# Optimization experiments

Hardware: AMD Instinct MI355X
Metric: run time of the kernel (lower is better)

Reference implementation:

```python
import jax, jax.numpy as jnp
import numpy as np

N = 100000   # nodes
E = 800000   # edges (avg degree 8)
IN = 128     # in_dim
H = 128      # hidden_dim
L = 3        # num_layers
EPS = 1e-5   # torch LayerNorm default


def setup_inputs() -> dict:
    key = jax.random.key(0)
    ks = jax.random.split(key, 10)
    s = 0.05
    # DAG edge list: src < dst guarantees acyclicity and node N-1 is a sink.
    rng = np.random.default_rng(0)
    src = rng.integers(0, N - 1, size=E)
    dst = src + 1 + (rng.random(E) * (N - 1 - src)).astype(np.int64)
    return {
        "node_feats": jax.random.normal(ks[0], (N, IN), jnp.float32),
        "src": jnp.asarray(src, jnp.int32),
        "dst": jnp.asarray(dst, jnp.int32),
        "W_in": jax.random.normal(ks[1], (IN, H), jnp.float32) * s,
        "b_in": jnp.zeros((H,), jnp.float32),
        "Ws": jax.random.normal(ks[2], (L, H, H), jnp.float32) * s,
        "bs": jnp.zeros((L, H), jnp.float32),
        "Wn": jax.random.normal(ks[3], (L, H, H), jnp.float32) * s,
        "bn": jnp.zeros((L, H), jnp.float32),
        "Wg": jax.random.normal(ks[4], (L, 2 * H, H), jnp.float32) * s,
        "bg": jnp.zeros((L, H), jnp.float32),
        "gamma": jnp.ones((L, H), jnp.float32),
        "beta": jnp.zeros((L, H), jnp.float32),
        "W_att": jax.random.normal(ks[5], (H, H), jnp.float32) * s,
        "b_att": jnp.zeros((H,), jnp.float32),
        "W_score": jax.random.normal(ks[6], (H, 1), jnp.float32) * s,
        "b_score": jnp.zeros((1,), jnp.float32),
    }


def reference(node_feats, src, dst, W_in, b_in, Ws, bs, Wn, bn, Wg, bg,
              gamma, beta, W_att, b_att, W_score, b_score):
    n = node_feats.shape[0]
    ones_e = jnp.ones(src.shape, node_feats.dtype)
    indeg = jax.ops.segment_sum(ones_e, dst, num_segments=n)          # [N]
    has_pred = (indeg > 0).astype(node_feats.dtype)[:, None]          # [N,1]
    inv_deg = (1.0 / jnp.maximum(indeg, 1.0))[:, None]                # [N,1]
    outdeg = jax.ops.segment_sum(ones_e, src, num_segments=n)
    sink_mask = outdeg == 0                                           # [N]

    h = node_feats @ W_in + b_in                                      # [N,H]
    for i in range(Ws.shape[0]):
        hs = h @ Ws[i] + bs[i]
        # predecessor mean of layer-input h (no within-layer recurrence)
        neigh = jax.ops.segment_sum(h[src], dst, num_segments=n) * inv_deg
        hn = neigh @ Wn[i] + bn[i]
        m = hs + has_pred * hn  # nodes with no preds use m = hs only (bias too)
        gate = jax.nn.sigmoid(jnp.concatenate([h, m], axis=-1) @ Wg[i] + bg[i])
        v = gate * m + (1.0 - gate) * h
        mu = v.mean(-1, keepdims=True)
        var = ((v - mu) ** 2).mean(-1, keepdims=True)
        v = (v - mu) * jax.lax.rsqrt(var + EPS) * gamma[i] + beta[i]
        h = jax.nn.relu(v)

    # attention pooling over sink nodes only
    a = jnp.tanh(h @ W_att + b_att)
    scores = (a @ W_score)[:, 0] + b_score[0]
    scores = jnp.where(sink_mask, scores, -jnp.inf)
    w = jax.nn.softmax(scores, axis=0)  # zero weight on non-sinks
    graph_emb = (w[:, None] * h).sum(0)
    return h, graph_emb
```

## Files before the change

kernel.cpp:

```cpp
#include <hip/hip_runtime.h>
#include <cmath>

typedef unsigned short u16;
typedef unsigned int   u32;
typedef __attribute__((ext_vector_type(8))) short bf16x8;
typedef __attribute__((ext_vector_type(4))) float f32x4;
typedef __attribute__((ext_vector_type(4))) u32   u32x4;

__device__ __forceinline__ float bf2f(u16 u){
    union { u32 i; float f; } x; x.i = ((u32)u) << 16; return x.f;
}
__device__ __forceinline__ u16 f2bf(float f){
    union { float f; u32 i; } x; x.f = f;
    u32 r = x.i + 0x7fffu + ((x.i >> 16) & 1u);
    return (u16)(r >> 16);
}


__global__ void k_count(const int* __restrict__ src, const int* __restrict__ dst,
                        int* cnt, int* notsink, int* pos, int E){
    int e = blockIdx.x*256 + threadIdx.x;
    if (e < E){
        pos[e] = atomicAdd(&cnt[dst[e]], 1);
        notsink[src[e]] = 1;
    }
}

__global__ void k_scan1(const int* __restrict__ in, int* blocksum, int N){
    __shared__ int sh[256];
    int tid = threadIdx.x;
    int base = blockIdx.x*1024 + tid*4;
    int s = 0;
    for (int j=0;j<4;j++){ int i = base+j; s += (i < N) ? in[i] : 0; }
    sh[tid] = s; __syncthreads();
    for (int d=128; d>0; d>>=1){ if (tid < d) sh[tid] += sh[tid+d]; __syncthreads(); }
    if (tid == 0) blocksum[blockIdx.x] = sh[0];
}

__global__ void k_scan2(int* blocksum, int nb){
    if (threadIdx.x == 0){
        int run = 0;
        for (int i=0;i<nb;i++){ int v = blocksum[i]; blocksum[i] = run; run += v; }
    }
}

__global__ void k_scan3(const int* __restrict__ in, const int* __restrict__ blockoff,
                        int* out, float* inv_deg, float* haspred, int N){
    __shared__ int sh[256];
    int tid = threadIdx.x;
    int base = blockIdx.x*1024 + tid*4;
    int e[4]; int s = 0;
    for (int j=0;j<4;j++){ int i = base+j; e[j] = (i < N) ? in[i] : 0; s += e[j]; }
    sh[tid] = s; __syncthreads();
    for (int d=1; d<256; d<<=1){
        int t = (tid >= d) ? sh[tid-d] : 0;
        __syncthreads();
        sh[tid] += t;
        __syncthreads();
    }
    int excl = sh[tid] - s + blockoff[blockIdx.x];
    for (int j=0;j<4;j++){
        int i = base+j;
        if (i < N){
            out[i] = excl; excl += e[j];
            inv_deg[i] = 1.0f / (float)(e[j] > 1 ? e[j] : 1);
            haspred[i] = e[j] > 0 ? 1.0f : 0.0f;
        }
    }
}

__global__ void k_place(const int* __restrict__ src, const int* __restrict__ dst,
                        const int* __restrict__ row_ptr, const int* __restrict__ pos,
                        int* csr_src, int E){
    int e = blockIdx.x*256 + threadIdx.x;
    if (e < E)
        csr_src[row_ptr[dst[e]] + pos[e]] = src[e];
}

__global__ void k_wt(const float* __restrict__ in, u16* __restrict__ out,
                     int shift, int K, int total){
    int i = blockIdx.x*256 + threadIdx.x;
    if (i < total){
        int mat = i >> shift;
        int within = i & ((1 << shift) - 1);
        int k = within >> 7, n = within & 127;
        out[(size_t)mat*(K*128) + n*K + k] = f2bf(in[i]);
    }
}


__global__ void k_neigh(const u16* __restrict__ h, const int* __restrict__ row_ptr,
                        const int* __restrict__ indeg, const float* __restrict__ inv_deg,
                        const int* __restrict__ csr_src, u16* __restrict__ neigh, int N){
    int wid  = (blockIdx.x*256 + threadIdx.x) >> 6;
    int lane = threadIdx.x & 63;
    int sub = lane >> 4, sl = lane & 15;
    int node = wid*4 + sub;
    bool valid = node < N;
    int deg   = valid ? indeg[node]   : 0;
    int start = valid ? row_ptr[node] : 0;
    float acc[8] = {0.f,0.f,0.f,0.f,0.f,0.f,0.f,0.f};
    for (int e0 = 0; __any(e0 < deg); e0 += 16){
        int idx = 0;
        if (e0 + sl < deg) idx = csr_src[start + e0 + sl];
        int cnt = deg - e0;
        #pragma unroll
        for (int j = 0; j < 16; j++){
            int sidx = __shfl(idx, (sub << 4) | j);
            if (j < cnt){
                bf16x8 v = *(const bf16x8*)(h + (size_t)sidx*128 + sl*8);
                #pragma unroll
                for (int t=0;t<8;t++) acc[t] += bf2f((u16)v[t]);
            }
        }
    }
    if (valid){
        float iv = inv_deg[node];
        u16 o[8];
        #pragma unroll
        for (int t=0;t<8;t++) o[t] = f2bf(acc[t]*iv);
        *(u32x4*)(neigh + (size_t)node*128 + sl*8) = *(const u32x4*)o;
    }
}


__device__ __forceinline__ void stage_A_bf16(const u16* __restrict__ A, u16 (*lA)[136],
                                             int row0, int n_rows, int tid){
    #pragma unroll
    for (int i=0;i<4;i++){
        int c = i*256 + tid;
        int r = c >> 4, col8 = (c & 15) * 8;
        u32x4 v = {0,0,0,0};
        if (row0 + r < n_rows)
            v = *(const u32x4*)(A + (size_t)(row0 + r)*128 + col8);
        *(u32x4*)&lA[r][col8] = v;
    }
}

__device__ __forceinline__ void stage_A_f32(const float* __restrict__ A, u16 (*lA)[136],
                                            int row0, int n_rows, int tid){
    #pragma unroll
    for (int i=0;i<4;i++){
        int c = i*256 + tid;
        int r = c >> 4, col8 = (c & 15) * 8;
        u16 o[8] = {0,0,0,0,0,0,0,0};
        if (row0 + r < n_rows){
            float4 v0 = *(const float4*)(A + (size_t)(row0 + r)*128 + col8);
            float4 v1 = *(const float4*)(A + (size_t)(row0 + r)*128 + col8 + 4);
            o[0]=f2bf(v0.x); o[1]=f2bf(v0.y); o[2]=f2bf(v0.z); o[3]=f2bf(v0.w);
            o[4]=f2bf(v1.x); o[5]=f2bf(v1.y); o[6]=f2bf(v1.z); o[7]=f2bf(v1.w);
        }
        *(u32x4*)&lA[r][col8] = *(const u32x4*)o;
    }
}

__device__ __forceinline__ void stage_B(const u16* __restrict__ BT, int Ks, int koff0,
                                        u16 (*lB)[136], int tid){
    #pragma unroll
    for (int i=0;i<8;i++){
        int c = i*256 + tid;
        int n = c >> 4, col8 = (c & 15) * 8;
        u32x4 v = *(const u32x4*)(BT + (size_t)n*Ks + koff0 + col8);
        *(u32x4*)&lB[n][col8] = v;
    }
}

__device__ __forceinline__ void stage_B_half(const u16* __restrict__ BT, int Ks, int koff0,
                                             u16 (*lB)[72], int tid){
    #pragma unroll
    for (int i=0;i<4;i++){
        int c = i*256 + tid;
        int n = c >> 3, col8 = (c & 7) * 8;
        *(u32x4*)&lB[n][col8] = *(const u32x4*)(BT + (size_t)n*Ks + koff0 + col8);
    }
}

__device__ __forceinline__ void mfma_tile(const u16 (*lA)[136], const u16 (*lB)[136],
                                          int wave, int lane, f32x4* acc){
    #pragma unroll
    for (int kk=0;kk<4;kk++){
        int koff = kk*32 + (lane >> 4) * 8;
        bf16x8 a = *(const bf16x8*)&lA[wave*16 + (lane & 15)][koff];
        #pragma unroll
        for (int t=0;t<8;t++){
            bf16x8 b = *(const bf16x8*)&lB[t*16 + (lane & 15)][koff];
            acc[t] = __builtin_amdgcn_mfma_f32_16x16x32_bf16(a, b, acc[t], 0, 0, 0);
        }
    }
}

__device__ __forceinline__ void mfma_half(const u16 (*lA)[136], const u16 (*lB)[72],
                                          int wave, int lane, int kbaseA, f32x4* acc){
    #pragma unroll
    for (int kk=0;kk<2;kk++){
        int kw = kk*32 + (lane >> 4) * 8;
        bf16x8 a = *(const bf16x8*)&lA[wave*16 + (lane & 15)][kbaseA + kw];
        #pragma unroll
        for (int t=0;t<8;t++){
            bf16x8 b = *(const bf16x8*)&lB[t*16 + (lane & 15)][kw];
            acc[t] = __builtin_amdgcn_mfma_f32_16x16x32_bf16(a, b, acc[t], 0, 0, 0);
        }
    }
}


__global__ __launch_bounds__(256) void k_gemm_in(
    const float* __restrict__ A, const u16* __restrict__ BT,
    const float* __restrict__ bias, u16* __restrict__ C, int n_rows)
{
    __shared__ u16 lA[64][136];
    __shared__ u16 lB[128][136];
    int tid = threadIdx.x, wave = tid >> 6, lane = tid & 63;
    int row0 = blockIdx.x * 64;
    f32x4 acc[8];
    #pragma unroll
    for (int t=0;t<8;t++) acc[t] = (f32x4){0.f,0.f,0.f,0.f};
    stage_A_f32(A, lA, row0, n_rows, tid);
    stage_B(BT, 128, 0, lB, tid);
    __syncthreads();
    mfma_tile(lA, lB, wave, lane, acc);

    int sl = lane & 15;
    int rbase = wave*16 + (lane >> 4)*4;
    float bc[8];
    #pragma unroll
    for (int t=0;t<8;t++) bc[t] = bias[t*16 + sl];
    for (int r=0;r<4;r++){
        int row = row0 + rbase + r;
        if (row >= n_rows) continue;
        #pragma unroll
        for (int t=0;t<8;t++)
            C[(size_t)row*128 + t*16 + sl] = f2bf(acc[t][r] + bc[t]);
    }
}


__global__ __launch_bounds__(256) void k_layer(
    const u16* __restrict__ H, const u16* __restrict__ Ng,
    const u16* __restrict__ BsT, const u16* __restrict__ BnT,
    const u16* __restrict__ BgT,
    const float* __restrict__ bs, const float* __restrict__ bn,
    const float* __restrict__ bg,
    const float* __restrict__ gamma, const float* __restrict__ beta,
    const float* __restrict__ haspred,
    u16* __restrict__ Hb, float* __restrict__ Hf, int n_rows)
{
    __shared__ u16 lA[64][136];
    __shared__ u16 lM[64][136];
    __shared__ u16 lB[128][72];
    int tid = threadIdx.x, wave = tid >> 6, lane = tid & 63;
    int sl = lane & 15;
    int row0 = blockIdx.x * 64;
    f32x4 accs[8], accn[8];
    #pragma unroll
    for (int t=0;t<8;t++){ accs[t] = (f32x4){0.f,0.f,0.f,0.f}; accn[t] = (f32x4){0.f,0.f,0.f,0.f}; }

    stage_A_bf16(H, lA, row0, n_rows, tid);
    stage_B_half(BsT, 128, 0, lB, tid);
    __syncthreads();
    mfma_half(lA, lB, wave, lane, 0, accs);
    __syncthreads();
    stage_B_half(BsT, 128, 64, lB, tid);
    __syncthreads();
    mfma_half(lA, lB, wave, lane, 64, accs);
    __syncthreads();

    stage_A_bf16(Ng, lM, row0, n_rows, tid);
    stage_B_half(BnT, 128, 0, lB, tid);
    __syncthreads();
    mfma_half(lM, lB, wave, lane, 0, accn);
    __syncthreads();
    stage_B_half(BnT, 128, 64, lB, tid);
    __syncthreads();
    mfma_half(lM, lB, wave, lane, 64, accn);
    __syncthreads();

    int rbase = wave*16 + (lane >> 4)*4;
    {
        float bsc[8], bnc[8];
        #pragma unroll
        for (int t=0;t<8;t++){ bsc[t] = bs[t*16 + sl]; bnc[t] = bn[t*16 + sl]; }
        #pragma unroll
        for (int r=0;r<4;r++){
            int row = row0 + rbase + r;
            float hp = (row < n_rows) ? haspred[row] : 0.f;
            #pragma unroll
            for (int t=0;t<8;t++){
                float m = accs[t][r] + bsc[t] + hp*(accn[t][r] + bnc[t]);
                lM[rbase + r][t*16 + sl] = f2bf(m);
            }
        }
    }
    __syncthreads();

    #pragma unroll
    for (int t=0;t<8;t++) accs[t] = (f32x4){0.f,0.f,0.f,0.f};
    stage_B_half(BgT, 256, 0, lB, tid);
    __syncthreads();
    mfma_half(lA, lB, wave, lane, 0, accs);
    __syncthreads();
    stage_B_half(BgT, 256, 64, lB, tid);
    __syncthreads();
    mfma_half(lA, lB, wave, lane, 64, accs);
    __syncthreads();
    stage_B_half(BgT, 256, 128, lB, tid);
    __syncthreads();
    mfma_half(lM, lB, wave, lane, 0, accs);
    __syncthreads();
    stage_B_half(BgT, 256, 192, lB, tid);
    __syncthreads();
    mfma_half(lM, lB, wave, lane, 64, accs);
    __syncthreads();

    float bgc[8], gam[8], bet[8];
    #pragma unroll
    for (int t=0;t<8;t++){
        int col = t*16 + sl;
        bgc[t] = bg[col]; gam[t] = gamma[col]; bet[t] = beta[col];
    }
    for (int r=0;r<4;r++){
        int row = row0 + rbase + r;
        if (row >= n_rows) continue;
        float v[8], s = 0.f;
        #pragma unroll
        for (int t=0;t<8;t++){
            int col = t*16 + sl;
            float x = accs[t][r] + bgc[t];
            float g = 1.f/(1.f + expf(-x));
            float hv = bf2f(H[(size_t)row*128 + col]);
            float mv = bf2f(lM[rbase + r][col]);
            v[t] = g*mv + (1.f - g)*hv;
            s += v[t];
        }
        s += __shfl_xor(s,1); s += __shfl_xor(s,2); s += __shfl_xor(s,4); s += __shfl_xor(s,8);
        float mu = s * (1.f/128.f);
        float q = 0.f;
        #pragma unroll
        for (int t=0;t<8;t++){ float d = v[t]-mu; q += d*d; }
        q += __shfl_xor(q,1); q += __shfl_xor(q,2); q += __shfl_xor(q,4); q += __shfl_xor(q,8);
        float rs = rsqrtf(q*(1.f/128.f) + 1e-5f);
        #pragma unroll
        for (int t=0;t<8;t++){
            size_t idx = (size_t)row*128 + t*16 + sl;
            float o = (v[t]-mu)*rs*gam[t] + bet[t];
            o = o > 0.f ? o : 0.f;
            Hb[idx] = f2bf(o);
            if (Hf) Hf[idx] = o;
        }
    }
}


__global__ __launch_bounds__(256) void k_gemm_att(
    const u16* __restrict__ H, const u16* __restrict__ BT,
    const float* __restrict__ b_att, const float* __restrict__ Wsc,
    const float* __restrict__ bsc, const int* __restrict__ notsink,
    float* __restrict__ scores, int n_rows)
{
    __shared__ u16 lA[64][136];
    __shared__ u16 lB[128][136];
    int tid = threadIdx.x, wave = tid >> 6, lane = tid & 63;
    int row0 = blockIdx.x * 64;
    f32x4 acc[8];
    #pragma unroll
    for (int t=0;t<8;t++) acc[t] = (f32x4){0.f,0.f,0.f,0.f};
    stage_A_bf16(H, lA, row0, n_rows, tid);
    stage_B(BT, 128, 0, lB, tid);
    __syncthreads();
    mfma_tile(lA, lB, wave, lane, acc);

    int sl = lane & 15;
    int rbase = wave*16 + (lane >> 4)*4;
    float bac[8], wc[8];
    #pragma unroll
    for (int t=0;t<8;t++){ bac[t] = b_att[t*16 + sl]; wc[t] = Wsc[t*16 + sl]; }
    float b0 = bsc[0];
    for (int r=0;r<4;r++){
        int row = row0 + rbase + r;
        if (row >= n_rows) continue;
        float p = 0.f;
        #pragma unroll
        for (int t=0;t<8;t++) p += tanhf(acc[t][r] + bac[t]) * wc[t];
        p += __shfl_xor(p,1); p += __shfl_xor(p,2); p += __shfl_xor(p,4); p += __shfl_xor(p,8);
        if (sl == 0)
            scores[row] = (notsink[row] == 0) ? (p + b0) : -INFINITY;
    }
}


__global__ void k_sum1(const float* __restrict__ scores, float* part, int N){
    __shared__ float sh[256];
    int tid = threadIdx.x;
    float s = 0.f;
    for (int i = blockIdx.x*256 + tid; i < N; i += 256*256) s += expf(scores[i]);
    sh[tid] = s; __syncthreads();
    for (int d=128; d>0; d>>=1){ if (tid < d) sh[tid] += sh[tid+d]; __syncthreads(); }
    if (tid == 0) part[blockIdx.x] = sh[0];
}

__global__ void k_sum2(const float* __restrict__ part, float* invsum){
    __shared__ float sh[256];
    int tid = threadIdx.x;
    sh[tid] = part[tid]; __syncthreads();
    for (int d=128; d>0; d>>=1){ if (tid < d) sh[tid] += sh[tid+d]; __syncthreads(); }
    if (tid == 0) invsum[0] = 1.f / sh[0];
}

__global__ void k_emb1(const u16* __restrict__ h, const float* __restrict__ scores,
                       float* accum, int N){
    __shared__ float sh[256];
    int tid = threadIdx.x;
    int col = tid & 127, grp = tid >> 7;
    float acc = 0.f;
    for (int n = blockIdx.x*2 + grp; n < N; n += 512){
        float s = scores[n];
        if (s > -1e30f){
            float w = expf(s);
            acc += w * bf2f(h[(size_t)n*128 + col]);
        }
    }
    sh[tid] = acc; __syncthreads();
    if (tid < 128) atomicAdd(&accum[col], sh[tid] + sh[tid+128]);
}

__global__ void k_emb2(const float* __restrict__ accum, const float* __restrict__ invsum,
                       float* __restrict__ out){
    int c = threadIdx.x;
    if (c < 128) out[c] = accum[c] * invsum[0];
}


extern "C" void kernel_launch(void* const* d_in, const int* in_sizes, int n_in,
                              void* d_out, int out_size, void* d_ws, size_t ws_size,
                              hipStream_t stream)
{
    const float* node_feats = (const float*)d_in[0];
    const int* src     = (const int*)d_in[1];
    const int* dst     = (const int*)d_in[2];
    const float* W_in    = (const float*)d_in[3];
    const float* b_in    = (const float*)d_in[4];
    const float* Ws      = (const float*)d_in[5];
    const float* bs      = (const float*)d_in[6];
    const float* Wn      = (const float*)d_in[7];
    const float* bn      = (const float*)d_in[8];
    const float* Wg      = (const float*)d_in[9];
    const float* bg      = (const float*)d_in[10];
    const float* gamma   = (const float*)d_in[11];
    const float* beta    = (const float*)d_in[12];
    const float* W_att   = (const float*)d_in[13];
    const float* b_att   = (const float*)d_in[14];
    const float* W_score = (const float*)d_in[15];
    const float* b_score = (const float*)d_in[16];

    const int N = in_sizes[0] / 128;
    const int E = in_sizes[1];

    char* w = (char*)d_ws;
    auto alloc = [&](size_t bytes)->char* {
        char* p = w; w += (bytes + 255) & ~(size_t)255; return p;
    };
    u16* WT_in  = (u16*)alloc(128*128*2);
    u16* WT_s   = (u16*)alloc(3*128*128*2);
    u16* WT_n   = (u16*)alloc(3*128*128*2);
    u16* WT_g   = (u16*)alloc(3*128*256*2);
    u16* WT_att = (u16*)alloc(128*128*2);
    int* cnt      = (int*)alloc((size_t)N*4);
    int* notsink  = (int*)alloc((size_t)N*4);
    float* emb_accum = (float*)alloc(128*4);
    size_t zero_bytes = (size_t)((char*)(emb_accum + 128) - (char*)cnt);
    int* pos      = (int*)alloc((size_t)E*4);
    int* row_ptr  = (int*)alloc((size_t)N*4);
    int* blocksum = (int*)alloc(1024*4);
    int* csr_src  = (int*)alloc((size_t)E*4);
    float* inv_deg = (float*)alloc((size_t)N*4);
    float* haspred = (float*)alloc((size_t)N*4);
    float* scores  = (float*)alloc((size_t)N*4);
    float* part    = (float*)alloc(256*4);
    float* invsum  = (float*)alloc(256);
    u16* buf_h = (u16*)alloc((size_t)N*128*2);
    u16* buf_b = (u16*)alloc((size_t)N*128*2);

    float* h_out   = (float*)d_out;
    float* emb_out = h_out + (size_t)N*128;

    hipMemsetAsync(cnt, 0, zero_bytes, stream);

    k_wt<<<(16384+255)/256, 256, 0, stream>>>(W_in,  WT_in,  14, 128, 16384);
    k_wt<<<(49152+255)/256, 256, 0, stream>>>(Ws,    WT_s,   14, 128, 49152);
    k_wt<<<(49152+255)/256, 256, 0, stream>>>(Wn,    WT_n,   14, 128, 49152);
    k_wt<<<(98304+255)/256, 256, 0, stream>>>(Wg,    WT_g,   15, 256, 98304);
    k_wt<<<(16384+255)/256, 256, 0, stream>>>(W_att, WT_att, 14, 128, 16384);

    k_count<<<(E+255)/256, 256, 0, stream>>>(src, dst, cnt, notsink, pos, E);

    int nb = (N + 1023) / 1024;
    k_scan1<<<nb, 256, 0, stream>>>(cnt, blocksum, N);
    k_scan2<<<1, 256, 0, stream>>>(blocksum, nb);
    k_scan3<<<nb, 256, 0, stream>>>(cnt, blocksum, row_ptr, inv_deg, haspred, N);
    k_place<<<(E+255)/256, 256, 0, stream>>>(src, dst, row_ptr, pos, csr_src, E);

    int gblk = (N + 63) / 64;
    int nblk = (N + 15) / 16;

    k_gemm_in<<<gblk, 256, 0, stream>>>(node_feats, WT_in, b_in, buf_h, N);

    for (int i=0;i<3;i++){
        k_neigh<<<nblk, 256, 0, stream>>>(buf_h, row_ptr, cnt, inv_deg, csr_src, buf_b, N);
        float* f32out = (i == 2) ? h_out : nullptr;
        k_layer<<<gblk, 256, 0, stream>>>(buf_h, buf_b,
                                          WT_s + i*16384, WT_n + i*16384, WT_g + i*32768,
                                          bs + i*128, bn + i*128, bg + i*128,
                                          gamma + i*128, beta + i*128, haspred,
                                          buf_h, f32out, N);
    }

    k_gemm_att<<<gblk, 256, 0, stream>>>(buf_h, WT_att, b_att, W_score, b_score,
                                         notsink, scores, N);
    k_sum1<<<256, 256, 0, stream>>>(scores, part, N);
    k_sum2<<<1, 256, 0, stream>>>(part, invsum);
    k_emb1<<<256, 256, 0, stream>>>(buf_h, scores, emb_accum, N);
    k_emb2<<<1, 128, 0, stream>>>(emb_accum, invsum, emb_out);

    (void)n_in; (void)out_size; (void)ws_size;
}
```

Baseline: 627.6 us.

## Merge weight-transpose launches, fuse pooling kernels, ping-pong h buffers, read h from LDS

The five weight-transpose launches become one kernel. The softmax-sum and weighted-embedding passes are fused into one pass that accumulates both, which cuts four pooling kernels to two. The layer kernel now reads the residual h from the already staged LDS tile instead of global memory, and one barrier is dropped. Layers ping-pong between two h buffers so the kernel no longer overwrites its own input, which removes a read/write race across blocks.

```diff
diff --git a/kernel.cpp b/kernel.cpp
--- a/kernel.cpp
+++ b/kernel.cpp
@@ -77,15 +77,22 @@
         csr_src[row_ptr[dst[e]] + pos[e]] = src[e];
 }
 
-__global__ void k_wt(const float* __restrict__ in, u16* __restrict__ out,
-                     int shift, int K, int total){
+__global__ void k_wt_all(const float* __restrict__ W_in, const float* __restrict__ Ws,
+                         const float* __restrict__ Wn, const float* __restrict__ Wg,
+                         const float* __restrict__ W_att,
+                         u16* WT_in, u16* WT_s, u16* WT_n, u16* WT_g, u16* WT_att){
     int i = blockIdx.x*256 + threadIdx.x;
-    if (i < total){
-        int mat = i >> shift;
-        int within = i & ((1 << shift) - 1);
-        int k = within >> 7, n = within & 127;
-        out[(size_t)mat*(K*128) + n*K + k] = f2bf(in[i]);
-    }
+    const float* src; u16* dst; int shift, K, off;
+    if (i < 16384)      { src=W_in;  dst=WT_in;  shift=14; K=128; off=i; }
+    else if (i < 65536) { src=Ws;    dst=WT_s;   shift=14; K=128; off=i-16384; }
+    else if (i < 114688){ src=Wn;    dst=WT_n;   shift=14; K=128; off=i-65536; }
+    else if (i < 212992){ src=Wg;    dst=WT_g;   shift=15; K=256; off=i-114688; }
+    else if (i < 229376){ src=W_att; dst=WT_att; shift=14; K=128; off=i-212992; }
+    else return;
+    int mat = off >> shift;
+    int w = off & ((1 << shift) - 1);
+    int k = w >> 7, n = w & 127;
+    dst[(size_t)mat*(K*128) + n*K + k] = f2bf(src[off]);
 }
 
 
@@ -249,7 +256,7 @@
     __shared__ u16 lM[64][136];
     __shared__ u16 lB[128][72];
     int tid = threadIdx.x, wave = tid >> 6, lane = tid & 63;
-    int sl = lane & 15;
+    int sl = lane & 15, g16 = lane >> 4;
     int row0 = blockIdx.x * 64;
     f32x4 accs[8], accn[8];
     #pragma unroll
@@ -275,7 +282,7 @@
     mfma_half(lM, lB, wave, lane, 64, accn);
     __syncthreads();
 
-    int rbase = wave*16 + (lane >> 4)*4;
+    int rbase = wave*16 + g16*4;
     {
         float bsc[8], bnc[8];
         #pragma unroll
@@ -310,7 +317,6 @@
     stage_B_half(BgT, 256, 192, lB, tid);
     __syncthreads();
     mfma_half(lM, lB, wave, lane, 64, accs);
-    __syncthreads();
 
     float bgc[8], gam[8], bet[8];
     #pragma unroll
@@ -326,10 +332,10 @@
         for (int t=0;t<8;t++){
             int col = t*16 + sl;
             float x = accs[t][r] + bgc[t];
-            float g = 1.f/(1.f + expf(-x));
-            float hv = bf2f(H[(size_t)row*128 + col]);
+            float gg = 1.f/(1.f + expf(-x));
+            float hv = bf2f(lA[rbase + r][col]);
             float mv = bf2f(lM[rbase + r][col]);
-            v[t] = g*mv + (1.f - g)*hv;
+            v[t] = gg*mv + (1.f - gg)*hv;
             s += v[t];
         }
         s += __shfl_xor(s,1); s += __shfl_xor(s,2); s += __shfl_xor(s,4); s += __shfl_xor(s,8);
@@ -388,45 +394,36 @@
 }
 
 
-__global__ void k_sum1(const float* __restrict__ scores, float* part, int N){
+__global__ void k_pool1(const u16* __restrict__ h, const float* __restrict__ scores,
+                        float* accum, float* part, int N){
     __shared__ float sh[256];
-    int tid = threadIdx.x;
-    float s = 0.f;
-    for (int i = blockIdx.x*256 + tid; i < N; i += 256*256) s += expf(scores[i]);
-    sh[tid] = s; __syncthreads();
-    for (int d=128; d>0; d>>=1){ if (tid < d) sh[tid] += sh[tid+d]; __syncthreads(); }
-    if (tid == 0) part[blockIdx.x] = sh[0];
-}
-
-__global__ void k_sum2(const float* __restrict__ part, float* invsum){
-    __shared__ float sh[256];
-    int tid = threadIdx.x;
-    sh[tid] = part[tid]; __syncthreads();
-    for (int d=128; d>0; d>>=1){ if (tid < d) sh[tid] += sh[tid+d]; __syncthreads(); }
-    if (tid == 0) invsum[0] = 1.f / sh[0];
-}
-
-__global__ void k_emb1(const u16* __restrict__ h, const float* __restrict__ scores,
-                       float* accum, int N){
-    __shared__ float sh[256];
+    __shared__ float sw[256];
     int tid = threadIdx.x;
     int col = tid & 127, grp = tid >> 7;
-    float acc = 0.f;
+    float acc = 0.f, wsum = 0.f;
     for (int n = blockIdx.x*2 + grp; n < N; n += 512){
         float s = scores[n];
         if (s > -1e30f){
             float w = expf(s);
             acc += w * bf2f(h[(size_t)n*128 + col]);
-        }
-    }
-    sh[tid] = acc; __syncthreads();
+            if (col == 0) wsum += w;
+        }
+    }
+    sh[tid] = acc; sw[tid] = wsum; __syncthreads();
+    if (tid < 128) sw[tid] += sw[tid+128];
+    __syncthreads();
+    for (int d=64; d>0; d>>=1){ if (tid < d) sw[tid] += sw[tid+d]; __syncthreads(); }
     if (tid < 128) atomicAdd(&accum[col], sh[tid] + sh[tid+128]);
-}
-
-__global__ void k_emb2(const float* __restrict__ accum, const float* __restrict__ invsum,
-                       float* __restrict__ out){
-    int c = threadIdx.x;
-    if (c < 128) out[c] = accum[c] * invsum[0];
+    if (tid == 0) part[blockIdx.x] = sw[0];
+}
+
+__global__ void k_pool2(const float* __restrict__ part, const float* __restrict__ accum,
+                        float* __restrict__ out){
+    __shared__ float sh[256];
+    int tid = threadIdx.x;
+    sh[tid] = part[tid]; __syncthreads();
+    for (int d=128; d>0; d>>=1){ if (tid < d) sh[tid] += sh[tid+d]; __syncthreads(); }
+    if (tid < 128) out[tid] = accum[tid] / sh[0];
 }
 
 
@@ -476,20 +473,17 @@
     float* haspred = (float*)alloc((size_t)N*4);
     float* scores  = (float*)alloc((size_t)N*4);
     float* part    = (float*)alloc(256*4);
-    float* invsum  = (float*)alloc(256);
-    u16* buf_h = (u16*)alloc((size_t)N*128*2);
-    u16* buf_b = (u16*)alloc((size_t)N*128*2);
+    u16* buf0 = (u16*)alloc((size_t)N*128*2);
+    u16* buf1 = (u16*)alloc((size_t)N*128*2);
+    u16* bufn = (u16*)alloc((size_t)N*128*2);
 
     float* h_out   = (float*)d_out;
     float* emb_out = h_out + (size_t)N*128;
 
     hipMemsetAsync(cnt, 0, zero_bytes, stream);
 
-    k_wt<<<(16384+255)/256, 256, 0, stream>>>(W_in,  WT_in,  14, 128, 16384);
-    k_wt<<<(49152+255)/256, 256, 0, stream>>>(Ws,    WT_s,   14, 128, 49152);
-    k_wt<<<(49152+255)/256, 256, 0, stream>>>(Wn,    WT_n,   14, 128, 49152);
-    k_wt<<<(98304+255)/256, 256, 0, stream>>>(Wg,    WT_g,   15, 256, 98304);
-    k_wt<<<(16384+255)/256, 256, 0, stream>>>(W_att, WT_att, 14, 128, 16384);
+    k_wt_all<<<(229376+255)/256, 256, 0, stream>>>(W_in, Ws, Wn, Wg, W_att,
+                                                   WT_in, WT_s, WT_n, WT_g, WT_att);
 
     k_count<<<(E+255)/256, 256, 0, stream>>>(src, dst, cnt, notsink, pos, E);
 
@@ -502,24 +496,25 @@
     int gblk = (N + 63) / 64;
     int nblk = (N + 15) / 16;
 
-    k_gemm_in<<<gblk, 256, 0, stream>>>(node_feats, WT_in, b_in, buf_h, N);
-
+    k_gemm_in<<<gblk, 256, 0, stream>>>(node_feats, WT_in, b_in, buf0, N);
+
+    u16* hin = buf0;
     for (int i=0;i<3;i++){
-        k_neigh<<<nblk, 256, 0, stream>>>(buf_h, row_ptr, cnt, inv_deg, csr_src, buf_b, N);
-        float* f32out = (i == 2) ? h_out : nullptr;
-        k_layer<<<gblk, 256, 0, stream>>>(buf_h, buf_b,
+        k_neigh<<<nblk, 256, 0, stream>>>(hin, row_ptr, cnt, inv_deg, csr_src, bufn, N);
+        u16* hb  = (hin == buf0) ? buf1 : buf0;
+        float* hf = (i == 2) ? h_out : nullptr;
+        k_layer<<<gblk, 256, 0, stream>>>(hin, bufn,
                                           WT_s + i*16384, WT_n + i*16384, WT_g + i*32768,
                                           bs + i*128, bn + i*128, bg + i*128,
                                           gamma + i*128, beta + i*128, haspred,
-                                          buf_h, f32out, N);
-    }
-
-    k_gemm_att<<<gblk, 256, 0, stream>>>(buf_h, WT_att, b_att, W_score, b_score,
+                                          hb, hf, N);
+        hin = hb;
+    }
+
+    k_gemm_att<<<gblk, 256, 0, stream>>>(hin, WT_att, b_att, W_score, b_score,
                                          notsink, scores, N);
-    k_sum1<<<256, 256, 0, stream>>>(scores, part, N);
-    k_sum2<<<1, 256, 0, stream>>>(part, invsum);
-    k_emb1<<<256, 256, 0, stream>>>(buf_h, scores, emb_accum, N);
-    k_emb2<<<1, 128, 0, stream>>>(emb_accum, invsum, emb_out);
+    k_pool1<<<256, 256, 0, stream>>>(hin, scores, emb_accum, part, N);
+    k_pool2<<<1, 256, 0, stream>>>(part, emb_accum, emb_out);
 
     (void)n_in; (void)out_size; (void)ws_size;
 }
```

After: 622.4 us. No clear change (-0.8%).
